# Kernel tuning notes

Hardware: AMD Instinct MI355X
Metric: run time of the kernel (lower is better)

## Reference

```python
import jax, jax.numpy as jnp
import numpy as np

H = 512      # config.hidden_dim
N = 64       # batch
W = 512      # sentence length
K = 8        # decode steps = pointer_answers.size(1)
NEG_BIG = 1e10


def setup_inputs() -> dict:
    key = jax.random.key(0)
    ks = jax.random.split(key, 10)
    stdv = 1.0 / np.sqrt(H)
    u = lambda k_, shape, s: jax.random.uniform(k_, shape, jnp.float32, -s, s)
    return {
        "context": jax.random.normal(ks[0], (N, W, 2 * H), jnp.float32),
        "sentence_lens": jax.random.randint(ks[1], (N,), 1, W + 1),
        "pointer_answers": jax.random.randint(ks[2], (N, K), 0, W + 1),
        "V_w": u(ks[3], (H, 2 * H), 1.0 / np.sqrt(2 * H)),
        "W_w": u(ks[4], (H, H), stdv),
        "v": u(ks[5], (H,), stdv),
        "w_ih": u(ks[6], (3 * H, 2 * H), stdv),
        "w_hh": u(ks[7], (3 * H, H), stdv),
        "b_ih": u(ks[8], (3 * H,), stdv),
        "b_hh": u(ks[9], (3 * H,), stdv),
    }


def reference(context, sentence_lens, pointer_answers, V_w, W_w, v, w_ih, w_hh, b_ih, b_hh):
    n, w_len, two_h = context.shape
    h_dim = two_h // 2
    k = pointer_answers.shape[1]

    # encoder output permuted to (W, N, 2H)
    ctx = jnp.swapaxes(context, 0, 1)
    # faithful reproduction of: context_new[i] = (1 - (i >= lens+1)*1e10) * context[i]
    pos = jnp.arange(w_len)[:, None]                                  # (W, 1)
    factor = 1.0 - (pos >= sentence_lens[None, :] + 1).astype(context.dtype) * NEG_BIG  # (W, N)
    ctx_masked = ctx * factor[:, :, None]                             # (W, N, 2H)
    # appended zeros row -> (W+1, N, 2H)
    context_new = jnp.concatenate([ctx_masked, jnp.zeros((1, n, two_h), context.dtype)], axis=0)

    ctx_t = jnp.einsum('snd,hd->snh', context_new, V_w)               # (W+1, N, H) = V(context_new)

    h0 = jnp.zeros((n, h_dim), context.dtype)

    def step(h, _):
        f = jnp.tanh(ctx_t + (h @ W_w.T)[None])                       # (W+1, N, H)
        scores = jnp.einsum('snh,h->sn', f, v)                        # (W+1, N)
        beta = jax.nn.softmax(scores, axis=0)                         # softmax over positions
        aligned = jnp.einsum('sn,snd->nd', beta, context_new)         # (N, 2H)
        # torch GRUCell math
        gi = aligned @ w_ih.T + b_ih                                  # (N, 3H)
        gh = h @ w_hh.T + b_hh                                        # (N, 3H)
        ir, iz, inew = jnp.split(gi, 3, axis=1)
        hr, hz, hnew = jnp.split(gh, 3, axis=1)
        r = jax.nn.sigmoid(ir + hr)
        z = jax.nn.sigmoid(iz + hz)
        ncand = jnp.tanh(inew + r * hnew)
        h_new = (1.0 - z) * ncand + z * h
        return h_new, beta.T                                          # (N, W+1)

    _, betas = jax.lax.scan(step, h0, None, length=k)                 # (k, N, W+1)
    # torch: cat over steps then permute -> (N, k, W+1) -> (N*k, W+1)
    out = jnp.transpose(betas, (1, 0, 2)).reshape(n * k, w_len + 1)
    return out
```

## Files before the change

kernel.cpp:

```cpp
#include <hip/hip_runtime.h>

#define N_    64
#define W_    512
#define H_    512
#define S_    513
#define TWOH_ 1024
#define KS_   8
#define FIXCAP_ 131072

typedef short s16x8 __attribute__((ext_vector_type(8)));
typedef float f32x4 __attribute__((ext_vector_type(4)));
typedef _Float16 h16x8 __attribute__((ext_vector_type(8)));

__device__ __forceinline__ float tanh_fast(float x) {
  float xc = fminf(fmaxf(x, -15.0f), 15.0f);
  float e = __expf(2.0f * xc);
  return (e - 1.0f) / (e + 1.0f);
}
__device__ __forceinline__ float sigmoid_f(float x) {
  return 1.0f / (1.0f + __expf(-x));
}
__device__ __forceinline__ float wred_sum(float v) {
#pragma unroll
  for (int m = 32; m > 0; m >>= 1) v += __shfl_xor(v, m, 64);
  return v;
}
__device__ __forceinline__ float bf2f(unsigned short u) {
  return __uint_as_float(((unsigned)u) << 16);
}

__device__ __forceinline__ void gld_lds16(const void* g, void* s) {
  __builtin_amdgcn_global_load_lds((__attribute__((address_space(1))) void*)g,
                                   (__attribute__((address_space(3))) void*)s,
                                   16, 0, 0);
}

__global__ __launch_bounds__(256) void k_cvt2(
    const float4* __restrict__ xa, unsigned short* __restrict__ Ahi,
    unsigned short* __restrict__ Alo, const float4* __restrict__ xb,
    unsigned short* __restrict__ Bhi, unsigned short* __restrict__ Blo) {
  const int NA = 8388608;
  const int NT = NA + 131072;
  for (int i = blockIdx.x * 256 + threadIdx.x; i < NT; i += gridDim.x * 256) {
    bool isA = (i < NA);
    float4 v = isA ? xa[i] : xb[i - NA];
    float vs[4] = {v.x, v.y, v.z, v.w};
    unsigned short hb[4], lb[4];
#pragma unroll
    for (int j = 0; j < 4; ++j) {
      unsigned u = __float_as_uint(vs[j]);
      unsigned short h = (unsigned short)((u + 0x7FFFu + ((u >> 16) & 1u)) >> 16);
      float hf = __uint_as_float((unsigned)h << 16);
      float lf = vs[j] - hf;
      unsigned u2 = __float_as_uint(lf);
      unsigned short l = (unsigned short)((u2 + 0x7FFFu + ((u2 >> 16) & 1u)) >> 16);
      hb[j] = h; lb[j] = l;
    }
    ushort4 h4; h4.x = hb[0]; h4.y = hb[1]; h4.z = hb[2]; h4.w = hb[3];
    ushort4 l4; l4.x = lb[0]; l4.y = lb[1]; l4.z = lb[2]; l4.w = lb[3];
    if (isA) {
      ((ushort4*)Ahi)[i] = h4;
      ((ushort4*)Alo)[i] = l4;
    } else {
      ((ushort4*)Bhi)[i - NA] = h4;
      ((ushort4*)Blo)[i - NA] = l4;
    }
  }
}

__global__ __launch_bounds__(256, 2) void mfma_gemm(
    const unsigned short* __restrict__ Ahi, const unsigned short* __restrict__ Alo,
    const unsigned short* __restrict__ Bhi, const unsigned short* __restrict__ Blo,
    _Float16* __restrict__ C, const int* __restrict__ slens,
    const float* __restrict__ vvec, float* __restrict__ scores,
    int* __restrict__ fixcnt, int* __restrict__ fixlist) {
  __shared__ unsigned short sAh[4096], sAl[4096], sBh[4096], sBl[4096];
  int bid = blockIdx.x;
  int swz = (bid & 7) * 128 + (bid >> 3);
  int mt = swz >> 2, nt = swz & 3;
  int m0 = mt * 128, n0 = nt * 128;
  int tid = threadIdx.x;
  int wave = tid >> 6, lane = tid & 63;
  int wr = wave >> 1, wc = wave & 1;
  int fr = lane & 15, fq = lane >> 4;
  int rA = tid >> 2;
  int cA = (tid & 3) * 8;

  f32x4 acc[4][4] = {};

  const size_t a_row0 = (size_t)(m0 + rA) << 10;
  const size_t a_row1 = (size_t)(m0 + rA + 64) << 10;
  const size_t b_row0 = (size_t)(n0 + rA) << 10;
  const size_t b_row1 = (size_t)(n0 + rA + 64) << 10;
  const int wofs = wave << 9;

  for (int k0 = 0; k0 < 1024; k0 += 32) {
    int off = k0 + cA;
    gld_lds16(Ahi + a_row0 + off, sAh + wofs);
    gld_lds16(Ahi + a_row1 + off, sAh + 2048 + wofs);
    gld_lds16(Alo + a_row0 + off, sAl + wofs);
    gld_lds16(Alo + a_row1 + off, sAl + 2048 + wofs);
    gld_lds16(Bhi + b_row0 + off, sBh + wofs);
    gld_lds16(Bhi + b_row1 + off, sBh + 2048 + wofs);
    gld_lds16(Blo + b_row0 + off, sBl + wofs);
    gld_lds16(Blo + b_row1 + off, sBl + 2048 + wofs);
    __syncthreads();
    s16x8 ah[4], av[4], bh[4], bv[4];
#pragma unroll
    for (int m = 0; m < 4; ++m) {
      int ar = (wr * 64 + m * 16 + fr) * 32 + fq * 8;
      ah[m] = *(const s16x8*)(sAh + ar);
      av[m] = *(const s16x8*)(sAl + ar);
    }
#pragma unroll
    for (int n = 0; n < 4; ++n) {
      int br = (wc * 64 + n * 16 + fr) * 32 + fq * 8;
      bh[n] = *(const s16x8*)(sBh + br);
      bv[n] = *(const s16x8*)(sBl + br);
    }
#pragma unroll
    for (int m = 0; m < 4; ++m)
#pragma unroll
      for (int n = 0; n < 4; ++n) {
        acc[m][n] = __builtin_amdgcn_mfma_f32_16x16x32_bf16(ah[m], bh[n], acc[m][n], 0, 0, 0);
        acc[m][n] = __builtin_amdgcn_mfma_f32_16x16x32_bf16(ah[m], bv[n], acc[m][n], 0, 0, 0);
        acc[m][n] = __builtin_amdgcn_mfma_f32_16x16x32_bf16(av[m], bh[n], acc[m][n], 0, 0, 0);
      }
    __syncthreads();
  }

  const int n_batch = m0 >> 9;
  const int len = slens[n_batch];
  const int s_tile0 = m0 & 511;
  const bool any_masked = (s_tile0 + 127 >= len + 1);
  float vv4[4];
#pragma unroll
  for (int nf = 0; nf < 4; ++nf) vv4[nf] = vvec[n0 + wc * 64 + nf * 16 + fr];

#pragma unroll
  for (int m = 0; m < 4; ++m) {
    int gr0 = m0 + wr * 64 + m * 16 + fq * 4;
#pragma unroll
    for (int nf = 0; nf < 4; ++nf) {
      int gc = n0 + wc * 64 + nf * 16 + fr;
      _Float16* cp = C + (size_t)gr0 * 512 + gc;
#pragma unroll
      for (int r = 0; r < 4; ++r) cp[(size_t)r * 512] = (_Float16)acc[m][nf][r];
    }
    if (any_masked) {
#pragma unroll
      for (int r = 0; r < 4; ++r) {
        int s_row = (gr0 + r) & 511;
        if (s_row >= len + 1) {
          float part = 0.0f;
#pragma unroll
          for (int nf = 0; nf < 4; ++nf) {
            float a = acc[m][nf][r];
            if (fabsf(a) <= 1e-5f) {
              int gc = n0 + wc * 64 + nf * 16 + fr;
              int idx = atomicAdd(fixcnt, 1);
              if (idx < FIXCAP_) fixlist[idx] = (n_batch << 20) | (s_row << 10) | gc;
            } else {
              part += (a > 0.0f) ? -vv4[nf] : vv4[nf];
            }
          }
          part += __shfl_xor(part, 1, 64);
          part += __shfl_xor(part, 2, 64);
          part += __shfl_xor(part, 4, 64);
          part += __shfl_xor(part, 8, 64);
          if (fr == 0) atomicAdd(&scores[n_batch * S_ + s_row], part);
        }
      }
    }
  }
}

__global__ __launch_bounds__(256) void k_fix(
    const float* __restrict__ ctx, const float* __restrict__ Vw,
    const float* __restrict__ vvec, const int* __restrict__ fixcnt,
    const int* __restrict__ fixlist, float* __restrict__ scores) {
  int wid = (blockIdx.x * 256 + threadIdx.x) >> 6;
  int lane = threadIdx.x & 63;
  int cnt = min(*fixcnt, FIXCAP_);
  for (int e = wid; e < cnt; e += 1024) {
    int pk = fixlist[e];
    int n = pk >> 20, s = (pk >> 10) & 1023, h = pk & 1023;
    const float* cr = ctx + ((size_t)n * W_ + s) * TWOH_ + lane * 16;
    const float* wr = Vw + (size_t)h * TWOH_ + lane * 16;
    double acc = 0.0;
#pragma unroll
    for (int i = 0; i < 16; ++i) acc += (double)cr[i] * (double)wr[i];
#pragma unroll
    for (int m = 32; m > 0; m >>= 1) acc += __shfl_xor(acc, m, 64);
    if (lane == 0) {
      float vh = vvec[h];
      float contrib = (acc > 0.0) ? -vh : ((acc < 0.0) ? vh : 0.0f);
      if (contrib != 0.0f) atomicAdd(&scores[n * S_ + s], contrib);
    }
  }
}

__global__ __launch_bounds__(1024) void k_prep2(
    const float* __restrict__ ctx, const int* __restrict__ slens,
    const float* __restrict__ scores, float* __restrict__ Cmask) {
  __shared__ float4 red4[16 * 64];
  int nb = blockIdx.x & 63, cb = blockIdx.x >> 6;
  int t = threadIdx.x;
  int len = slens[nb];
  int dl = t & 63, sl = t >> 6;
  int d4 = cb * 256 + dl * 4;
  const float4* cp = (const float4*)(ctx + (size_t)nb * W_ * TWOH_) + (d4 >> 2);
  float4 acc = make_float4(0.f, 0.f, 0.f, 0.f);
#pragma unroll 4
  for (int s = len + 1 + sl; s < W_; s += 16) {
    float ew = __expf(scores[nb * S_ + s]);
    float4 c4 = cp[(size_t)s * (TWOH_ / 4)];
    acc.x += ew * c4.x; acc.y += ew * c4.y;
    acc.z += ew * c4.z; acc.w += ew * c4.w;
  }
  red4[sl * 64 + dl] = acc;
  __syncthreads();
  if (sl == 0) {
    float4 s4 = red4[dl];
#pragma unroll
    for (int i = 1; i < 16; ++i) {
      float4 o = red4[i * 64 + dl];
      s4.x += o.x; s4.y += o.y; s4.z += o.z; s4.w += o.w;
    }
    s4.x *= -1.0e10f; s4.y *= -1.0e10f; s4.z *= -1.0e10f; s4.w *= -1.0e10f;
    *(float4*)(Cmask + nb * TWOH_ + d4) = s4;
  }
}

__global__ __launch_bounds__(1024) void k_hw(const float* __restrict__ hc,
                                             const float* __restrict__ Ww,
                                             float* __restrict__ hWb) {
  __shared__ float ww[4][512];
  int b = blockIdx.x;
  int t = threadIdx.x;
  int h0 = b * 4;
  for (int i = t; i < 4 * 512; i += 1024)
    ww[i >> 9][i & 511] = Ww[(size_t)(h0 + (i >> 9)) * H_ + (i & 511)];
  __syncthreads();
  int lane = t & 63;
  int hl = (t >> 6) & 3;
  int nh = t >> 8;
  const float* wr = &ww[hl][lane << 3];
  float4 w0 = *(const float4*)wr;
  float4 w1 = *(const float4*)(wr + 4);
  for (int n = nh * 16; n < nh * 16 + 16; n += 2) {
    const float* hr0 = hc + (size_t)n * H_ + (lane << 3);
    const float* hr1 = hr0 + H_;
    float4 a0 = *(const float4*)hr0;
    float4 a1 = *(const float4*)(hr0 + 4);
    float4 b0 = *(const float4*)hr1;
    float4 b1 = *(const float4*)(hr1 + 4);
    float acc0 = a0.x * w0.x + a0.y * w0.y + a0.z * w0.z + a0.w * w0.w +
                 a1.x * w1.x + a1.y * w1.y + a1.z * w1.z + a1.w * w1.w;
    float acc1 = b0.x * w0.x + b0.y * w0.y + b0.z * w0.z + b0.w * w0.w +
                 b1.x * w1.x + b1.y * w1.y + b1.z * w1.z + b1.w * w1.w;
    acc0 = wred_sum(acc0);
    acc1 = wred_sum(acc1);
    if (lane == 0) {
      hWb[(size_t)n * H_ + h0 + hl] = acc0;
      hWb[(size_t)(n + 1) * H_ + h0 + hl] = acc1;
    }
  }
}

__global__ __launch_bounds__(1024) void k_scores(
    const int* __restrict__ slens, const float* __restrict__ hWb,
    const _Float16* __restrict__ Vc16, const float* __restrict__ vvec,
    float* __restrict__ scores) {
  int nb = blockIdx.x & 63, cb = blockIdx.x >> 6;
  int t = threadIdx.x;
  int len = slens[nb];
  int smax = min(len, W_ - 1);
  int w = t >> 6, lane = t & 63;
  int hb = lane << 3;
  float4 h0 = *(const float4*)(hWb + nb * H_ + hb);
  float4 h1 = *(const float4*)(hWb + nb * H_ + hb + 4);
  float4 v0 = *(const float4*)(vvec + hb);
  float4 v1 = *(const float4*)(vvec + hb + 4);
  float hw[8] = {h0.x, h0.y, h0.z, h0.w, h1.x, h1.y, h1.z, h1.w};
  float vv[8] = {v0.x, v0.y, v0.z, v0.w, v1.x, v1.y, v1.z, v1.w};
  int s_end = min((cb + 1) * 64 - 1, smax);
  const _Float16* vcb = Vc16 + (size_t)nb * W_ * H_ + hb;
  int s = cb * 64 + w;
  for (; s + 16 <= s_end; s += 32) {
    h16x8 x0 = *(const h16x8*)(vcb + (size_t)s * H_);
    h16x8 x1 = *(const h16x8*)(vcb + (size_t)(s + 16) * H_);
    float a0 = 0.f, a1 = 0.f;
#pragma unroll
    for (int i = 0; i < 8; ++i) {
      a0 += tanh_fast((float)x0[i] + hw[i]) * vv[i];
      a1 += tanh_fast((float)x1[i] + hw[i]) * vv[i];
    }
    a0 = wred_sum(a0); a1 = wred_sum(a1);
    if (lane == 0) {
      scores[nb * S_ + s] = a0;
      scores[nb * S_ + s + 16] = a1;
    }
  }
  for (; s <= s_end; s += 16) {
    h16x8 x8 = *(const h16x8*)(vcb + (size_t)s * H_);
    float acc = 0.0f;
#pragma unroll
    for (int i = 0; i < 8; ++i) acc += tanh_fast((float)x8[i] + hw[i]) * vv[i];
    acc = wred_sum(acc);
    if (lane == 0) scores[nb * S_ + s] = acc;
  }
  if (cb == 7 && w == 15) {
    float acc = 0.0f;
#pragma unroll
    for (int i = 0; i < 8; ++i) acc += tanh_fast(hw[i]) * vv[i];
    acc = wred_sum(acc);
    if (lane == 0) scores[nb * S_ + W_] = acc;
  }
}

__global__ __launch_bounds__(1024) void k_soft_aligned(
    const unsigned short* __restrict__ ctxb, const int* __restrict__ slens,
    const float* __restrict__ scores, const float* __restrict__ Cmask,
    float* __restrict__ alignedb, float* __restrict__ out, int k) {
  __shared__ float beta[520];
  __shared__ float wsum[16];
  __shared__ float redl[64 * 16 * 8];
  int nb = blockIdx.x & 63, cb = blockIdx.x >> 6;
  int t = threadIdx.x;
  int len = slens[nb];
  int smax = min(len, W_ - 1);

  float e = (t < S_) ? __expf(scores[nb * S_ + t]) : 0.0f;
  float ws_ = wred_sum(e);
  if ((t & 63) == 0) wsum[t >> 6] = ws_;
  __syncthreads();
  float D = 0.0f;
#pragma unroll
  for (int i = 0; i < 16; ++i) D += wsum[i];
  if (t < S_) {
    float bt = e / D;
    beta[t] = bt;
    if (cb == 0) out[(size_t)(nb * KS_ + k) * S_ + t] = bt;
  }
  __syncthreads();

  int dl = t & 15, sl = t >> 4;
  int d8 = cb * 128 + dl * 8;
  const unsigned short* cp = ctxb + (size_t)nb * W_ * TWOH_ + d8;
  float a[8] = {};
  int s = sl;
  for (; s + 64 <= smax; s += 128) {
    float b0 = beta[s], b1 = beta[s + 64];
    s16x8 c0 = *(const s16x8*)(cp + (size_t)s * TWOH_);
    s16x8 c1 = *(const s16x8*)(cp + (size_t)(s + 64) * TWOH_);
#pragma unroll
    for (int i = 0; i < 8; ++i)
      a[i] += b0 * bf2f((unsigned short)c0[i]) + b1 * bf2f((unsigned short)c1[i]);
  }
  for (; s <= smax; s += 64) {
    float bt = beta[s];
    s16x8 c = *(const s16x8*)(cp + (size_t)s * TWOH_);
#pragma unroll
    for (int i = 0; i < 8; ++i) a[i] += bt * bf2f((unsigned short)c[i]);
  }
  float4* rp = (float4*)(redl + sl * 128 + dl * 8);
  rp[0] = make_float4(a[0], a[1], a[2], a[3]);
  rp[1] = make_float4(a[4], a[5], a[6], a[7]);
  __syncthreads();
  if (t < 128) {
    float ssum = 0.0f;
#pragma unroll 16
    for (int q = 0; q < 64; ++q) ssum += redl[q * 128 + t];
    float coef = 1.0f / D;
    int dd = nb * TWOH_ + cb * 128 + t;
    alignedb[dd] = ssum + coef * Cmask[dd];
  }
}

__global__ __launch_bounds__(1024) void k_gru(
    const float* __restrict__ alignedb, const float* __restrict__ hc,
    const float* __restrict__ wih, const float* __restrict__ whh,
    const float* __restrict__ bih, const float* __restrict__ bhh,
    float* __restrict__ hnx) {
  __shared__ float ls_wih[6 * TWOH_];
  __shared__ float ls_whh[6 * H_];
  __shared__ float part[8 * 128 * 6];
  int b = blockIdx.x;
  int t = threadIdx.x;
  const int j0 = 2 * b;
  for (int i = t; i < 6 * TWOH_; i += 1024) {
    int row = i >> 10, d = i & 1023;
    int jl = row / 3, g = row - jl * 3;
    ls_wih[i] = wih[(size_t)(g * H_ + j0 + jl) * TWOH_ + d];
  }
  for (int i = t; i < 6 * H_; i += 1024) {
    int row = i >> 9, d = i & 511;
    int jl = row / 3, g = row - jl * 3;
    ls_whh[i] = whh[(size_t)(g * H_ + j0 + jl) * H_ + d];
  }
  __syncthreads();
  int nj = t & 127, sl = t >> 7;
  int n = nj & 63, jl = nj >> 6;
  const float* ar = alignedb + n * TWOH_ + sl * 128;
  const float* hr = hc + n * H_ + sl * 64;
  const float* w0 = ls_wih + (jl * 3 + 0) * TWOH_ + sl * 128;
  const float* w1 = ls_wih + (jl * 3 + 1) * TWOH_ + sl * 128;
  const float* w2 = ls_wih + (jl * 3 + 2) * TWOH_ + sl * 128;
  const float* u0 = ls_whh + (jl * 3 + 0) * H_ + sl * 64;
  const float* u1 = ls_whh + (jl * 3 + 1) * H_ + sl * 64;
  const float* u2 = ls_whh + (jl * 3 + 2) * H_ + sl * 64;
  float g0 = 0.f, g1 = 0.f, g2 = 0.f;
#pragma unroll 8
  for (int i = 0; i < 128; i += 4) {
    float4 a4 = *(const float4*)(ar + i);
    g0 += a4.x * w0[i] + a4.y * w0[i + 1] + a4.z * w0[i + 2] + a4.w * w0[i + 3];
    g1 += a4.x * w1[i] + a4.y * w1[i + 1] + a4.z * w1[i + 2] + a4.w * w1[i + 3];
    g2 += a4.x * w2[i] + a4.y * w2[i + 1] + a4.z * w2[i + 2] + a4.w * w2[i + 3];
  }
  float q0 = 0.f, q1 = 0.f, q2 = 0.f;
#pragma unroll 8
  for (int i = 0; i < 64; i += 4) {
    float4 h4 = *(const float4*)(hr + i);
    q0 += h4.x * u0[i] + h4.y * u0[i + 1] + h4.z * u0[i + 2] + h4.w * u0[i + 3];
    q1 += h4.x * u1[i] + h4.y * u1[i + 1] + h4.z * u1[i + 2] + h4.w * u1[i + 3];
    q2 += h4.x * u2[i] + h4.y * u2[i + 1] + h4.z * u2[i + 2] + h4.w * u2[i + 3];
  }
  float* pp = part + (sl * 128 + nj) * 6;
  pp[0] = g0; pp[1] = g1; pp[2] = g2; pp[3] = q0; pp[4] = q1; pp[5] = q2;
  __syncthreads();
  if (t < 128) {
    int n2 = t & 63, jl2 = t >> 6;
    int j = j0 + jl2;
    float G0 = 0.f, G1 = 0.f, G2 = 0.f, Q0 = 0.f, Q1 = 0.f, Q2 = 0.f;
#pragma unroll
    for (int s = 0; s < 8; ++s) {
      float* p = part + (s * 128 + t) * 6;
      G0 += p[0]; G1 += p[1]; G2 += p[2];
      Q0 += p[3]; Q1 += p[4]; Q2 += p[5];
    }
    float r = sigmoid_f(G0 + bih[j] + Q0 + bhh[j]);
    float z = sigmoid_f(G1 + bih[H_ + j] + Q1 + bhh[H_ + j]);
    float nc = tanh_fast(G2 + bih[2 * H_ + j] + r * (Q2 + bhh[2 * H_ + j]));
    hnx[n2 * H_ + j] = (1.0f - z) * nc + z * hc[n2 * H_ + j];
  }
}

extern "C" void kernel_launch(void* const* d_in, const int* in_sizes, int n_in,
                              void* d_out, int out_size, void* d_ws, size_t ws_size,
                              hipStream_t stream) {
  const float* ctx = (const float*)d_in[0];
  const int* slens = (const int*)d_in[1];
  const float* Vw = (const float*)d_in[3];
  const float* Ww = (const float*)d_in[4];
  const float* vvec = (const float*)d_in[5];
  const float* wih = (const float*)d_in[6];
  const float* whh = (const float*)d_in[7];
  const float* bih = (const float*)d_in[8];
  const float* bhh = (const float*)d_in[9];
  float* out = (float*)d_out;

  char* p = (char*)d_ws;
  _Float16* Vc16 = (_Float16*)p;      p += (size_t)N_ * W_ * H_ * 2;
  float* scores = (float*)p;          p += (size_t)N_ * S_ * 4;
  int* fixcnt = (int*)p;              p += 256;
  int* fixlist = (int*)p;             p += (size_t)FIXCAP_ * 4;
  float* Cm = (float*)p;              p += (size_t)N_ * TWOH_ * 4;
  float* hb = (float*)p;              p += (size_t)2 * N_ * H_ * 4;
  float* hWb = (float*)p;             p += (size_t)N_ * H_ * 4;
  float* al = (float*)p;              p += (size_t)N_ * TWOH_ * 4;
  unsigned short* Ahi = (unsigned short*)p;  p += (size_t)32768 * 1024 * 2;
  unsigned short* Alo = (unsigned short*)p;  p += (size_t)32768 * 1024 * 2;
  unsigned short* Bhi = (unsigned short*)p;  p += (size_t)512 * 1024 * 2;
  unsigned short* Blo = (unsigned short*)p;  p += (size_t)512 * 1024 * 2;
  size_t need = (size_t)(p - (char*)d_ws);
  if (ws_size < need) return;

  hipMemsetAsync(hb, 0, (size_t)N_ * H_ * sizeof(float), stream);
  hipMemsetAsync(fixcnt, 0, sizeof(int), stream);
  hipMemsetAsync(scores, 0, (size_t)N_ * S_ * sizeof(float), stream);
  k_cvt2<<<2048, 256, 0, stream>>>((const float4*)ctx, Ahi, Alo,
                                   (const float4*)Vw, Bhi, Blo);
  mfma_gemm<<<1024, 256, 0, stream>>>(Ahi, Alo, Bhi, Blo, Vc16, slens, vvec,
                                      scores, fixcnt, fixlist);
  k_fix<<<256, 256, 0, stream>>>(ctx, Vw, vvec, fixcnt, fixlist, scores);
  k_prep2<<<256, 1024, 0, stream>>>(ctx, slens, scores, Cm);

  for (int k = 0; k < KS_; ++k) {
    const float* hc = hb + (k & 1) * (N_ * H_);
    float* hn = hb + ((k + 1) & 1) * (N_ * H_);
    k_hw<<<128, 1024, 0, stream>>>(hc, Ww, hWb);
    k_scores<<<512, 1024, 0, stream>>>(slens, hWb, Vc16, vvec, scores);
    k_soft_aligned<<<512, 1024, 0, stream>>>(Ahi, slens, scores, Cm, al, out, k);
    k_gru<<<256, 1024, 0, stream>>>(al, hc, wih, whh, bih, bhh, hn);
  }
}
```

Before: 653.9 us.

## Switch context GEMM to single-pass fp16 and fuse hW into scores kernel

```diff
diff --git a/kernel.cpp b/kernel.cpp
--- a/kernel.cpp
+++ b/kernel.cpp
@@ -8,9 +8,9 @@
 #define KS_   8
 #define FIXCAP_ 131072
 
-typedef short s16x8 __attribute__((ext_vector_type(8)));
 typedef float f32x4 __attribute__((ext_vector_type(4)));
 typedef _Float16 h16x8 __attribute__((ext_vector_type(8)));
+typedef _Float16 h16x4 __attribute__((ext_vector_type(4)));
 
 __device__ __forceinline__ float tanh_fast(float x) {
   float xc = fminf(fmaxf(x, -15.0f), 15.0f);
@@ -25,9 +25,6 @@
   for (int m = 32; m > 0; m >>= 1) v += __shfl_xor(v, m, 64);
   return v;
 }
-__device__ __forceinline__ float bf2f(unsigned short u) {
-  return __uint_as_float(((unsigned)u) << 16);
-}
 
 __device__ __forceinline__ void gld_lds16(const void* g, void* s) {
   __builtin_amdgcn_global_load_lds((__attribute__((address_space(1))) void*)g,
@@ -36,45 +33,34 @@
 }
 
 __global__ __launch_bounds__(256) void k_cvt2(
-    const float4* __restrict__ xa, unsigned short* __restrict__ Ahi,
-    unsigned short* __restrict__ Alo, const float4* __restrict__ xb,
-    unsigned short* __restrict__ Bhi, unsigned short* __restrict__ Blo) {
+    const float4* __restrict__ xa, _Float16* __restrict__ A16,
+    const float4* __restrict__ xb, _Float16* __restrict__ B16,
+    const float4* __restrict__ xw, _Float16* __restrict__ W16) {
   const int NA = 8388608;
-  const int NT = NA + 131072;
+  const int NB = 131072;
+  const int NW = 65536;
+  const int NT = NA + NB + NW;
   for (int i = blockIdx.x * 256 + threadIdx.x; i < NT; i += gridDim.x * 256) {
-    bool isA = (i < NA);
-    float4 v = isA ? xa[i] : xb[i - NA];
-    float vs[4] = {v.x, v.y, v.z, v.w};
-    unsigned short hb[4], lb[4];
-#pragma unroll
-    for (int j = 0; j < 4; ++j) {
-      unsigned u = __float_as_uint(vs[j]);
-      unsigned short h = (unsigned short)((u + 0x7FFFu + ((u >> 16) & 1u)) >> 16);
-      float hf = __uint_as_float((unsigned)h << 16);
-      float lf = vs[j] - hf;
-      unsigned u2 = __float_as_uint(lf);
-      unsigned short l = (unsigned short)((u2 + 0x7FFFu + ((u2 >> 16) & 1u)) >> 16);
-      hb[j] = h; lb[j] = l;
-    }
-    ushort4 h4; h4.x = hb[0]; h4.y = hb[1]; h4.z = hb[2]; h4.w = hb[3];
-    ushort4 l4; l4.x = lb[0]; l4.y = lb[1]; l4.z = lb[2]; l4.w = lb[3];
-    if (isA) {
-      ((ushort4*)Ahi)[i] = h4;
-      ((ushort4*)Alo)[i] = l4;
-    } else {
-      ((ushort4*)Bhi)[i - NA] = h4;
-      ((ushort4*)Blo)[i - NA] = l4;
-    }
-  }
-}
-
-__global__ __launch_bounds__(256, 2) void mfma_gemm(
-    const unsigned short* __restrict__ Ahi, const unsigned short* __restrict__ Alo,
-    const unsigned short* __restrict__ Bhi, const unsigned short* __restrict__ Blo,
+    const float4* src;
+    _Float16* dst;
+    int j;
+    if (i < NA) { src = xa; dst = A16; j = i; }
+    else if (i < NA + NB) { src = xb; dst = B16; j = i - NA; }
+    else { src = xw; dst = W16; j = i - NA - NB; }
+    float4 v = src[j];
+    h16x4 o;
+    o[0] = (_Float16)v.x; o[1] = (_Float16)v.y;
+    o[2] = (_Float16)v.z; o[3] = (_Float16)v.w;
+    *(h16x4*)(dst + (size_t)4 * j) = o;
+  }
+}
+
+__global__ __launch_bounds__(256, 4) void mfma_gemm(
+    const _Float16* __restrict__ A16, const _Float16* __restrict__ B16,
     _Float16* __restrict__ C, const int* __restrict__ slens,
     const float* __restrict__ vvec, float* __restrict__ scores,
     int* __restrict__ fixcnt, int* __restrict__ fixlist) {
-  __shared__ unsigned short sAh[4096], sAl[4096], sBh[4096], sBl[4096];
+  __shared__ _Float16 sA[4096], sB[4096];
   int bid = blockIdx.x;
   int swz = (bid & 7) * 128 + (bid >> 3);
   int mt = swz >> 2, nt = swz & 3;
@@ -96,36 +82,23 @@
 
   for (int k0 = 0; k0 < 1024; k0 += 32) {
     int off = k0 + cA;
-    gld_lds16(Ahi + a_row0 + off, sAh + wofs);
-    gld_lds16(Ahi + a_row1 + off, sAh + 2048 + wofs);
-    gld_lds16(Alo + a_row0 + off, sAl + wofs);
-    gld_lds16(Alo + a_row1 + off, sAl + 2048 + wofs);
-    gld_lds16(Bhi + b_row0 + off, sBh + wofs);
-    gld_lds16(Bhi + b_row1 + off, sBh + 2048 + wofs);
-    gld_lds16(Blo + b_row0 + off, sBl + wofs);
-    gld_lds16(Blo + b_row1 + off, sBl + 2048 + wofs);
+    gld_lds16(A16 + a_row0 + off, sA + wofs);
+    gld_lds16(A16 + a_row1 + off, sA + 2048 + wofs);
+    gld_lds16(B16 + b_row0 + off, sB + wofs);
+    gld_lds16(B16 + b_row1 + off, sB + 2048 + wofs);
     __syncthreads();
-    s16x8 ah[4], av[4], bh[4], bv[4];
-#pragma unroll
-    for (int m = 0; m < 4; ++m) {
-      int ar = (wr * 64 + m * 16 + fr) * 32 + fq * 8;
-      ah[m] = *(const s16x8*)(sAh + ar);
-      av[m] = *(const s16x8*)(sAl + ar);
-    }
-#pragma unroll
-    for (int n = 0; n < 4; ++n) {
-      int br = (wc * 64 + n * 16 + fr) * 32 + fq * 8;
-      bh[n] = *(const s16x8*)(sBh + br);
-      bv[n] = *(const s16x8*)(sBl + br);
-    }
+    h16x8 af[4], bf[4];
 #pragma unroll
     for (int m = 0; m < 4; ++m)
-#pragma unroll
-      for (int n = 0; n < 4; ++n) {
-        acc[m][n] = __builtin_amdgcn_mfma_f32_16x16x32_bf16(ah[m], bh[n], acc[m][n], 0, 0, 0);
-        acc[m][n] = __builtin_amdgcn_mfma_f32_16x16x32_bf16(ah[m], bv[n], acc[m][n], 0, 0, 0);
-        acc[m][n] = __builtin_amdgcn_mfma_f32_16x16x32_bf16(av[m], bh[n], acc[m][n], 0, 0, 0);
-      }
+      af[m] = *(const h16x8*)(sA + (wr * 64 + m * 16 + fr) * 32 + fq * 8);
+#pragma unroll
+    for (int n = 0; n < 4; ++n)
+      bf[n] = *(const h16x8*)(sB + (wc * 64 + n * 16 + fr) * 32 + fq * 8);
+#pragma unroll
+    for (int m = 0; m < 4; ++m)
+#pragma unroll
+      for (int n = 0; n < 4; ++n)
+        acc[m][n] = __builtin_amdgcn_mfma_f32_16x16x32_f16(af[m], bf[n], acc[m][n], 0, 0, 0);
     __syncthreads();
   }
 
@@ -153,15 +126,24 @@
         int s_row = (gr0 + r) & 511;
         if (s_row >= len + 1) {
           float part = 0.0f;
+          unsigned rare = 0u;
 #pragma unroll
           for (int nf = 0; nf < 4; ++nf) {
             float a = acc[m][nf][r];
-            if (fabsf(a) <= 1e-5f) {
-              int gc = n0 + wc * 64 + nf * 16 + fr;
-              int idx = atomicAdd(fixcnt, 1);
-              if (idx < FIXCAP_) fixlist[idx] = (n_batch << 20) | (s_row << 10) | gc;
-            } else {
-              part += (a > 0.0f) ? -vv4[nf] : vv4[nf];
+            part += (a > 0.0f) ? -vv4[nf] : vv4[nf];
+            if (fabsf(a) <= 1.5e-3f) rare |= (1u << nf);
+          }
+          if (__any(rare != 0u)) {
+#pragma unroll
+            for (int nf = 0; nf < 4; ++nf) {
+              if (rare & (1u << nf)) {
+                float a = acc[m][nf][r];
+                int gc = n0 + wc * 64 + nf * 16 + fr;
+                int sgn = (a > 0.0f) ? 1 : 0;
+                int idx = atomicAdd(fixcnt, 1);
+                if (idx < FIXCAP_)
+                  fixlist[idx] = (n_batch << 19) | (s_row << 10) | (gc << 1) | sgn;
+              }
             }
           }
           part += __shfl_xor(part, 1, 64);
@@ -182,9 +164,9 @@
   int wid = (blockIdx.x * 256 + threadIdx.x) >> 6;
   int lane = threadIdx.x & 63;
   int cnt = min(*fixcnt, FIXCAP_);
-  for (int e = wid; e < cnt; e += 1024) {
+  for (int e = wid; e < cnt; e += 8192) {
     int pk = fixlist[e];
-    int n = pk >> 20, s = (pk >> 10) & 1023, h = pk & 1023;
+    int n = pk >> 19, s = (pk >> 10) & 511, h = (pk >> 1) & 511, sgn = pk & 1;
     const float* cr = ctx + ((size_t)n * W_ + s) * TWOH_ + lane * 16;
     const float* wr = Vw + (size_t)h * TWOH_ + lane * 16;
     double acc = 0.0;
@@ -194,8 +176,10 @@
     for (int m = 32; m > 0; m >>= 1) acc += __shfl_xor(acc, m, 64);
     if (lane == 0) {
       float vh = vvec[h];
-      float contrib = (acc > 0.0) ? -vh : ((acc < 0.0) ? vh : 0.0f);
-      if (contrib != 0.0f) atomicAdd(&scores[n * S_ + s], contrib);
+      float spec = sgn ? -vh : vh;
+      float tru = (acc > 0.0) ? -vh : ((acc < 0.0) ? vh : 0.0f);
+      float d = tru - spec;
+      if (d != 0.0f) atomicAdd(&scores[n * S_ + s], d);
     }
   }
 }
@@ -232,62 +216,44 @@
   }
 }
 
-__global__ __launch_bounds__(1024) void k_hw(const float* __restrict__ hc,
-                                             const float* __restrict__ Ww,
-                                             float* __restrict__ hWb) {
-  __shared__ float ww[4][512];
-  int b = blockIdx.x;
+__global__ __launch_bounds__(1024) void k_scores_hw(
+    const int* __restrict__ slens, const float* __restrict__ hc,
+    const _Float16* __restrict__ W16, const _Float16* __restrict__ Vc16,
+    const float* __restrict__ vvec, float* __restrict__ scores, int k) {
+  __shared__ float s_hW[512];
+  int n = blockIdx.x;
   int t = threadIdx.x;
-  int h0 = b * 4;
-  for (int i = t; i < 4 * 512; i += 1024)
-    ww[i >> 9][i & 511] = Ww[(size_t)(h0 + (i >> 9)) * H_ + (i & 511)];
-  __syncthreads();
-  int lane = t & 63;
-  int hl = (t >> 6) & 3;
-  int nh = t >> 8;
-  const float* wr = &ww[hl][lane << 3];
-  float4 w0 = *(const float4*)wr;
-  float4 w1 = *(const float4*)(wr + 4);
-  for (int n = nh * 16; n < nh * 16 + 16; n += 2) {
-    const float* hr0 = hc + (size_t)n * H_ + (lane << 3);
-    const float* hr1 = hr0 + H_;
-    float4 a0 = *(const float4*)hr0;
-    float4 a1 = *(const float4*)(hr0 + 4);
-    float4 b0 = *(const float4*)hr1;
-    float4 b1 = *(const float4*)(hr1 + 4);
-    float acc0 = a0.x * w0.x + a0.y * w0.y + a0.z * w0.z + a0.w * w0.w +
-                 a1.x * w1.x + a1.y * w1.y + a1.z * w1.z + a1.w * w1.w;
-    float acc1 = b0.x * w0.x + b0.y * w0.y + b0.z * w0.z + b0.w * w0.w +
-                 b1.x * w1.x + b1.y * w1.y + b1.z * w1.z + b1.w * w1.w;
-    acc0 = wred_sum(acc0);
-    acc1 = wred_sum(acc1);
-    if (lane == 0) {
-      hWb[(size_t)n * H_ + h0 + hl] = acc0;
-      hWb[(size_t)(n + 1) * H_ + h0 + hl] = acc1;
-    }
-  }
-}
-
-__global__ __launch_bounds__(1024) void k_scores(
-    const int* __restrict__ slens, const float* __restrict__ hWb,
-    const _Float16* __restrict__ Vc16, const float* __restrict__ vvec,
-    float* __restrict__ scores) {
-  int nb = blockIdx.x & 63, cb = blockIdx.x >> 6;
-  int t = threadIdx.x;
-  int len = slens[nb];
-  int smax = min(len, W_ - 1);
   int w = t >> 6, lane = t & 63;
   int hb = lane << 3;
-  float4 h0 = *(const float4*)(hWb + nb * H_ + hb);
-  float4 h1 = *(const float4*)(hWb + nb * H_ + hb + 4);
+
+  if (k == 0) {
+    if (t < 512) s_hW[t] = 0.0f;
+  } else {
+    float4 ha = *(const float4*)(hc + (size_t)n * H_ + hb);
+    float4 hbv = *(const float4*)(hc + (size_t)n * H_ + hb + 4);
+    float hx[8] = {ha.x, ha.y, ha.z, ha.w, hbv.x, hbv.y, hbv.z, hbv.w};
+    for (int o = w; o < 512; o += 16) {
+      h16x8 w8 = *(const h16x8*)(W16 + (size_t)o * H_ + hb);
+      float a = 0.0f;
+#pragma unroll
+      for (int i = 0; i < 8; ++i) a += hx[i] * (float)w8[i];
+      a = wred_sum(a);
+      if (lane == 0) s_hW[o] = a;
+    }
+  }
+  __syncthreads();
+
+  int len = slens[n];
+  int smax = min(len, W_ - 1);
+  float4 h0 = *(const float4*)(s_hW + hb);
+  float4 h1 = *(const float4*)(s_hW + hb + 4);
   float4 v0 = *(const float4*)(vvec + hb);
   float4 v1 = *(const float4*)(vvec + hb + 4);
   float hw[8] = {h0.x, h0.y, h0.z, h0.w, h1.x, h1.y, h1.z, h1.w};
   float vv[8] = {v0.x, v0.y, v0.z, v0.w, v1.x, v1.y, v1.z, v1.w};
-  int s_end = min((cb + 1) * 64 - 1, smax);
-  const _Float16* vcb = Vc16 + (size_t)nb * W_ * H_ + hb;
-  int s = cb * 64 + w;
-  for (; s + 16 <= s_end; s += 32) {
+  const _Float16* vcb = Vc16 + (size_t)n * W_ * H_ + hb;
+  int s = w;
+  for (; s + 16 <= smax; s += 32) {
     h16x8 x0 = *(const h16x8*)(vcb + (size_t)s * H_);
     h16x8 x1 = *(const h16x8*)(vcb + (size_t)(s + 16) * H_);
     float a0 = 0.f, a1 = 0.f;
@@ -298,29 +264,29 @@
     }
     a0 = wred_sum(a0); a1 = wred_sum(a1);
     if (lane == 0) {
-      scores[nb * S_ + s] = a0;
-      scores[nb * S_ + s + 16] = a1;
-    }
-  }
-  for (; s <= s_end; s += 16) {
+      scores[n * S_ + s] = a0;
+      scores[n * S_ + s + 16] = a1;
+    }
+  }
+  for (; s <= smax; s += 16) {
     h16x8 x8 = *(const h16x8*)(vcb + (size_t)s * H_);
     float acc = 0.0f;
 #pragma unroll
     for (int i = 0; i < 8; ++i) acc += tanh_fast((float)x8[i] + hw[i]) * vv[i];
     acc = wred_sum(acc);
-    if (lane == 0) scores[nb * S_ + s] = acc;
-  }
-  if (cb == 7 && w == 15) {
+    if (lane == 0) scores[n * S_ + s] = acc;
+  }
+  if (w == 15) {
     float acc = 0.0f;
 #pragma unroll
     for (int i = 0; i < 8; ++i) acc += tanh_fast(hw[i]) * vv[i];
     acc = wred_sum(acc);
-    if (lane == 0) scores[nb * S_ + W_] = acc;
+    if (lane == 0) scores[n * S_ + W_] = acc;
   }
 }
 
 __global__ __launch_bounds__(1024) void k_soft_aligned(
-    const unsigned short* __restrict__ ctxb, const int* __restrict__ slens,
+    const _Float16* __restrict__ ctx16, const int* __restrict__ slens,
     const float* __restrict__ scores, const float* __restrict__ Cmask,
     float* __restrict__ alignedb, float* __restrict__ out, int k) {
   __shared__ float beta[520];
@@ -347,22 +313,22 @@
 
   int dl = t & 15, sl = t >> 4;
   int d8 = cb * 128 + dl * 8;
-  const unsigned short* cp = ctxb + (size_t)nb * W_ * TWOH_ + d8;
+  const _Float16* cp = ctx16 + (size_t)nb * W_ * TWOH_ + d8;
   float a[8] = {};
   int s = sl;
   for (; s + 64 <= smax; s += 128) {
     float b0 = beta[s], b1 = beta[s + 64];
-    s16x8 c0 = *(const s16x8*)(cp + (size_t)s * TWOH_);
-    s16x8 c1 = *(const s16x8*)(cp + (size_t)(s + 64) * TWOH_);
+    h16x8 c0 = *(const h16x8*)(cp + (size_t)s * TWOH_);
+    h16x8 c1 = *(const h16x8*)(cp + (size_t)(s + 64) * TWOH_);
 #pragma unroll
     for (int i = 0; i < 8; ++i)
-      a[i] += b0 * bf2f((unsigned short)c0[i]) + b1 * bf2f((unsigned short)c1[i]);
+      a[i] += b0 * (float)c0[i] + b1 * (float)c1[i];
   }
   for (; s <= smax; s += 64) {
     float bt = beta[s];
-    s16x8 c = *(const s16x8*)(cp + (size_t)s * TWOH_);
-#pragma unroll
-    for (int i = 0; i < 8; ++i) a[i] += bt * bf2f((unsigned short)c[i]);
+    h16x8 c = *(const h16x8*)(cp + (size_t)s * TWOH_);
+#pragma unroll
+    for (int i = 0; i < 8; ++i) a[i] += bt * (float)c[i];
   }
   float4* rp = (float4*)(redl + sl * 128 + dl * 8);
   rp[0] = make_float4(a[0], a[1], a[2], a[3]);
@@ -467,31 +433,28 @@
   int* fixlist = (int*)p;             p += (size_t)FIXCAP_ * 4;
   float* Cm = (float*)p;              p += (size_t)N_ * TWOH_ * 4;
   float* hb = (float*)p;              p += (size_t)2 * N_ * H_ * 4;
-  float* hWb = (float*)p;             p += (size_t)N_ * H_ * 4;
   float* al = (float*)p;              p += (size_t)N_ * TWOH_ * 4;
-  unsigned short* Ahi = (unsigned short*)p;  p += (size_t)32768 * 1024 * 2;
-  unsigned short* Alo = (unsigned short*)p;  p += (size_t)32768 * 1024 * 2;
-  unsigned short* Bhi = (unsigned short*)p;  p += (size_t)512 * 1024 * 2;
-  unsigned short* Blo = (unsigned short*)p;  p += (size_t)512 * 1024 * 2;
+  _Float16* A16 = (_Float16*)p;       p += (size_t)32768 * 1024 * 2;
+  _Float16* B16 = (_Float16*)p;       p += (size_t)512 * 1024 * 2;
+  _Float16* W16 = (_Float16*)p;       p += (size_t)512 * 512 * 2;
   size_t need = (size_t)(p - (char*)d_ws);
   if (ws_size < need) return;
 
   hipMemsetAsync(hb, 0, (size_t)N_ * H_ * sizeof(float), stream);
   hipMemsetAsync(fixcnt, 0, sizeof(int), stream);
   hipMemsetAsync(scores, 0, (size_t)N_ * S_ * sizeof(float), stream);
-  k_cvt2<<<2048, 256, 0, stream>>>((const float4*)ctx, Ahi, Alo,
-                                   (const float4*)Vw, Bhi, Blo);
-  mfma_gemm<<<1024, 256, 0, stream>>>(Ahi, Alo, Bhi, Blo, Vc16, slens, vvec,
-                                      scores, fixcnt, fixlist);
-  k_fix<<<256, 256, 0, stream>>>(ctx, Vw, vvec, fixcnt, fixlist, scores);
+  k_cvt2<<<2048, 256, 0, stream>>>((const float4*)ctx, A16, (const float4*)Vw,
+                                   B16, (const float4*)Ww, W16);
+  mfma_gemm<<<1024, 256, 0, stream>>>(A16, B16, Vc16, slens, vvec, scores,
+                                      fixcnt, fixlist);
+  k_fix<<<2048, 256, 0, stream>>>(ctx, Vw, vvec, fixcnt, fixlist, scores);
   k_prep2<<<256, 1024, 0, stream>>>(ctx, slens, scores, Cm);
 
   for (int k = 0; k < KS_; ++k) {
     const float* hc = hb + (k & 1) * (N_ * H_);
     float* hn = hb + ((k + 1) & 1) * (N_ * H_);
-    k_hw<<<128, 1024, 0, stream>>>(hc, Ww, hWb);
-    k_scores<<<512, 1024, 0, stream>>>(slens, hWb, Vc16, vvec, scores);
-    k_soft_aligned<<<512, 1024, 0, stream>>>(Ahi, slens, scores, Cm, al, out, k);
+    k_scores_hw<<<64, 1024, 0, stream>>>(slens, hc, W16, Vc16, vvec, scores, k);
+    k_soft_aligned<<<512, 1024, 0, stream>>>(A16, slens, scores, Cm, al, out, k);
     k_gru<<<256, 1024, 0, stream>>>(al, hc, wih, whh, bih, bhh, hn);
   }
 }
```

Result: slower. 1.098 ms (+68.0%).
